# Performance work log

Hardware: AMD Instinct MI355X
Metric: run time of the kernel (lower is better)

The kernel has to match this reference:

```python
import jax, jax.numpy as jnp
import numpy as np

EPS = 1e-06


def setup_inputs() -> dict:
    key = jax.random.key(0)
    ks = jax.random.split(key, 8)
    B, L, n, C = 4, 4096, 4, 1024
    D = n * C
    x = jax.random.normal(ks[0], (B, L, n, C), dtype=jnp.float32)
    # learned params (phi_* are zero-init in the module; use small random for a
    # non-trivial correctness baseline)
    norm_w = jnp.ones((D,), dtype=jnp.float32)
    W_pre = 0.02 * jax.random.normal(ks[1], (n, D), dtype=jnp.float32)
    W_post = 0.02 * jax.random.normal(ks[2], (n, D), dtype=jnp.float32)
    W_res = 0.02 * jax.random.normal(ks[3], (n * n, D), dtype=jnp.float32)
    b_pre = jnp.ones((n,), dtype=jnp.float32) / n
    b_post = jnp.ones((n,), dtype=jnp.float32)
    b_res = jnp.zeros((n, n), dtype=jnp.float32)
    alpha_pre = jnp.float32(0.01)
    alpha_post = jnp.float32(0.01)
    alpha_res = jnp.float32(0.01)
    return {"x": x, "norm_w": norm_w, "W_pre": W_pre, "W_post": W_post,
            "W_res": W_res, "b_pre": b_pre, "b_post": b_post, "b_res": b_res,
            "alpha_pre": alpha_pre, "alpha_post": alpha_post, "alpha_res": alpha_res}


def _cayley(M):
    # M: [N, n, n] -> orthogonal Q = (I - S)^{-1} (I + S), S skew-symmetric part
    S = 0.5 * (M - jnp.swapaxes(M, -1, -2))
    I = jnp.eye(M.shape[-1], dtype=M.dtype)
    return jnp.linalg.solve(I - S, I + S)


def reference(x, norm_w, W_pre, W_post, W_res, b_pre, b_post, b_res,
              alpha_pre, alpha_post, alpha_res):
    B, L, n, C = x.shape
    xf = x.reshape(B * L, n * C)
    # RMSNorm over n*C
    rms = jnp.sqrt(jnp.mean(xf * xf, axis=-1, keepdims=True) + EPS)
    xn = (xf / rms) * norm_w
    # tiny projections
    H_pre = jax.nn.sigmoid(alpha_pre * (xn @ W_pre.T) + b_pre)          # [BL, n]
    H_post = 2.0 * jax.nn.sigmoid(alpha_post * (xn @ W_post.T) + b_post)  # [BL, n]
    M = (alpha_res * (xn @ W_res.T)).reshape(B * L, n, n) + b_res
    H_res = _cayley(M).reshape(B, L, n, n)
    H_pre = H_pre.reshape(B, L, n)
    H_post = H_post.reshape(B, L, n)
    # pre-mapping: aggregate streams -> [B, L, C]
    y = jnp.einsum('bln,blnc->blc', H_pre, x)
    z = y  # identity sublayer
    # post-mapping: distribute back to streams
    o = H_post[..., None] * z[:, :, None, :]                             # [B,L,n,C]
    # residual mapping: orthogonal stream mixing
    r = jnp.einsum('blmn,blnc->blmc', H_res, x)
    return r + o
```

## Files before the change

### kernel.cpp

```cpp
#include <hip/hip_runtime.h>
#include <math.h>

#define DTOT   4096
#define NTOK   16384
#define NJ     24
#define NG     25
#define DC     256
#define NCHUNK (DTOT / DC)
#define TOKB   256

__global__ void prep_kernel(const float* __restrict__ Wpre,
                            const float* __restrict__ Wpost,
                            const float* __restrict__ Wres,
                            const float* __restrict__ nw,
                            float* __restrict__ Wt) {
    int i = blockIdx.x * 256 + threadIdx.x;
    if (i >= DTOT * NJ) return;
    int d = i / NJ;
    int j = i - d * NJ;
    float w;
    if (j < 4)       w = Wpre [(size_t)j       * DTOT + d];
    else if (j < 8)  w = Wpost[(size_t)(j - 4) * DTOT + d];
    else             w = Wres [(size_t)(j - 8) * DTOT + d];
    Wt[i] = w * nw[d];
}

__global__ __launch_bounds__(256) void dots_kernel(
        const float* __restrict__ x,
        const float* __restrict__ Wt,
        float* __restrict__ Gpart) {
    __shared__ float wlds[DC * NJ];

    const int tid = threadIdx.x;
    const int tg  = blockIdx.x;
    const int ch  = blockIdx.y;

    {
        const float4* src = (const float4*)(Wt + (size_t)ch * DC * NJ);
        float4* dst = (float4*)wlds;
        #pragma unroll
        for (int i = 0; i < (DC * NJ / 4) / 256; ++i)
            dst[tid + 256 * i] = src[tid + 256 * i];
    }
    __syncthreads();

    const int tok = tg * TOKB + tid;
    const float4* __restrict__ x0 =
        (const float4*)(x + (size_t)tok * DTOT + (size_t)ch * DC);

    float acc[NG];
    #pragma unroll
    for (int j = 0; j < NG; ++j) acc[j] = 0.f;

    for (int dd4 = 0; dd4 < DC / 4; ++dd4) {
        float4 r = x0[dd4];
        float a[4] = { r.x, r.y, r.z, r.w };
        #pragma unroll
        for (int k = 0; k < 4; ++k) {
            const float xa = a[k];
            const float4* __restrict__ wv =
                (const float4*)(wlds + (dd4 * 4 + k) * NJ);
            #pragma unroll
            for (int jv = 0; jv < 6; ++jv) {
                const float4 w = wv[jv];
                acc[4*jv+0] += xa * w.x;
                acc[4*jv+1] += xa * w.y;
                acc[4*jv+2] += xa * w.z;
                acc[4*jv+3] += xa * w.w;
            }
            acc[NG-1] += xa * xa;
        }
    }

    float* gp = Gpart + (size_t)ch * NG * NTOK;
    #pragma unroll
    for (int j = 0; j < NG; ++j)
        gp[(size_t)j * NTOK + tok] = acc[j];
}

__global__ __launch_bounds__(256) void out_kernel(
        const float* __restrict__ x,
        const float* __restrict__ Gpart,
        const float* __restrict__ bpre,
        const float* __restrict__ bpost,
        const float* __restrict__ bres,
        const float* __restrict__ apre,
        const float* __restrict__ apost,
        const float* __restrict__ ares,
        float* __restrict__ out) {
    const int lane  = threadIdx.x & 63;
    const int token = blockIdx.x * 4 + (threadIdx.x >> 6);

    float s = 0.f;
    if (lane < NG) {
        const float* gp = Gpart + (size_t)lane * NTOK + token;
        #pragma unroll
        for (int c = 0; c < NCHUNK; ++c)
            s += gp[(size_t)c * NG * NTOK];
    }

    float g[NG];
    #pragma unroll
    for (int j = 0; j < NG; ++j) g[j] = __shfl(s, j, 64);

    const float inv = rsqrtf(g[NG-1] * (1.0f / DTOT) + 1e-6f);
    const float a_pre  = apre[0];
    const float a_post = apost[0];
    const float a_res  = ares[0];

    float hpre[4], hpost[4];
    #pragma unroll
    for (int i = 0; i < 4; ++i) {
        float z1 = a_pre  * g[i]     * inv + bpre[i];
        hpre[i]  = 1.f / (1.f + expf(-z1));
        float z2 = a_post * g[4 + i] * inv + bpost[i];
        hpost[i] = 2.f / (1.f + expf(-z2));
    }

    float M[4][4];
    #pragma unroll
    for (int i = 0; i < 4; ++i)
        #pragma unroll
        for (int j = 0; j < 4; ++j)
            M[i][j] = a_res * g[8 + i * 4 + j] * inv + bres[i * 4 + j];

    float A[4][8];
    #pragma unroll
    for (int i = 0; i < 4; ++i)
        #pragma unroll
        for (int j = 0; j < 4; ++j) {
            float S = 0.5f * (M[i][j] - M[j][i]);
            float I = (i == j) ? 1.f : 0.f;
            A[i][j]     = I - S;
            A[i][4 + j] = I + S;
        }
    #pragma unroll
    for (int k = 0; k < 4; ++k) {
        float pv = 1.f / A[k][k];
        #pragma unroll
        for (int c = 0; c < 8; ++c) A[k][c] *= pv;
        #pragma unroll
        for (int i = 0; i < 4; ++i) {
            if (i == k) continue;
            float f = A[i][k];
            #pragma unroll
            for (int c = 0; c < 8; ++c) A[i][c] -= f * A[k][c];
        }
    }
    float cf[16];
    #pragma unroll
    for (int m = 0; m < 4; ++m)
        #pragma unroll
        for (int n = 0; n < 4; ++n)
            cf[m * 4 + n] = A[m][4 + n] + hpost[m] * hpre[n];

    const float* xt = x + (size_t)token * DTOT;
    float* ot = out + (size_t)token * DTOT;

    #pragma unroll
    for (int cc = 0; cc < 4; ++cc) {
        const int c0 = cc * 256 + lane * 4;
        float4 xv[4];
        #pragma unroll
        for (int n = 0; n < 4; ++n)
            xv[n] = *(const float4*)(xt + n * 1024 + c0);
        #pragma unroll
        for (int m = 0; m < 4; ++m) {
            float4 o;
            o.x = cf[m*4+0] * xv[0].x; o.y = cf[m*4+0] * xv[0].y;
            o.z = cf[m*4+0] * xv[0].z; o.w = cf[m*4+0] * xv[0].w;
            #pragma unroll
            for (int n = 1; n < 4; ++n) {
                const float c = cf[m * 4 + n];
                o.x += c * xv[n].x;
                o.y += c * xv[n].y;
                o.z += c * xv[n].z;
                o.w += c * xv[n].w;
            }
            *(float4*)(ot + m * 1024 + c0) = o;
        }
    }
}

extern "C" void kernel_launch(void* const* d_in, const int* in_sizes, int n_in,
                              void* d_out, int out_size, void* d_ws, size_t ws_size,
                              hipStream_t stream) {
    const float* x     = (const float*)d_in[0];
    const float* nw    = (const float*)d_in[1];
    const float* Wpre  = (const float*)d_in[2];
    const float* Wpost = (const float*)d_in[3];
    const float* Wres  = (const float*)d_in[4];
    const float* bpre  = (const float*)d_in[5];
    const float* bpost = (const float*)d_in[6];
    const float* bres  = (const float*)d_in[7];
    const float* apre  = (const float*)d_in[8];
    const float* apost = (const float*)d_in[9];
    const float* ares  = (const float*)d_in[10];
    float* out = (float*)d_out;

    float* Wt    = (float*)d_ws;
    float* Gpart = (float*)((char*)d_ws + (size_t)DTOT * NJ * sizeof(float));

    prep_kernel<<<(DTOT * NJ + 255) / 256, 256, 0, stream>>>(Wpre, Wpost, Wres, nw, Wt);

    dim3 ga(NTOK / TOKB, NCHUNK);
    dots_kernel<<<ga, 256, 0, stream>>>(x, Wt, Gpart);

    out_kernel<<<NTOK / 4, 256, 0, stream>>>(x, Gpart, bpre, bpost, bres,
                                             apre, apost, ares, out);
}
```

Before: 593.5 us.

## Compute two tokens per thread in dots kernel with prefetch and larger out blocks

The dots kernel now has each thread accumulate projections for two tokens, so every LDS weight load feeds twice as many FMAs. It also prefetches the next x vectors one step ahead, and uses a smaller feature chunk with a larger token block. The out kernel runs 16 tokens per 1024-thread block and switches to fast __expf. The smaller chunk doubles the number of partial sums written to and reduced from Gpart, which grows workspace and reduction traffic. The extra accumulators add register pressure.

```diff
diff --git a/kernel.cpp b/kernel.cpp
--- a/kernel.cpp
+++ b/kernel.cpp
@@ -5,9 +5,9 @@
 #define NTOK   16384
 #define NJ     24
 #define NG     25
-#define DC     256
+#define DC     128
 #define NCHUNK (DTOT / DC)
-#define TOKB   256
+#define TOKB   512
 
 __global__ void prep_kernel(const float* __restrict__ Wpre,
                             const float* __restrict__ Wpost,
@@ -25,7 +25,7 @@
     Wt[i] = w * nw[d];
 }
 
-__global__ __launch_bounds__(256) void dots_kernel(
+__global__ __launch_bounds__(256, 4) void dots_kernel(
         const float* __restrict__ x,
         const float* __restrict__ Wt,
         float* __restrict__ Gpart) {
@@ -44,41 +44,62 @@
     }
     __syncthreads();
 
-    const int tok = tg * TOKB + tid;
+    const int tok0 = tg * TOKB + tid;
+    const int tok1 = tok0 + 256;
     const float4* __restrict__ x0 =
-        (const float4*)(x + (size_t)tok * DTOT + (size_t)ch * DC);
-
-    float acc[NG];
-    #pragma unroll
-    for (int j = 0; j < NG; ++j) acc[j] = 0.f;
-
-    for (int dd4 = 0; dd4 < DC / 4; ++dd4) {
-        float4 r = x0[dd4];
-        float a[4] = { r.x, r.y, r.z, r.w };
-        #pragma unroll
-        for (int k = 0; k < 4; ++k) {
-            const float xa = a[k];
+        (const float4*)(x + (size_t)tok0 * DTOT + (size_t)ch * DC);
+    const float4* __restrict__ x1 =
+        (const float4*)(x + (size_t)tok1 * DTOT + (size_t)ch * DC);
+
+    float pa[NG], pb[NG];
+    #pragma unroll
+    for (int j = 0; j < NG; ++j) { pa[j] = 0.f; pb[j] = 0.f; }
+
+    float4 a0 = x0[0], a1 = x0[1];
+    float4 b0 = x1[0], b1 = x1[1];
+
+    for (int g = 0; g < DC / 8; ++g) {
+        float4 na0 = a0, na1 = a1, nb0 = b0, nb1 = b1;
+        if (g < DC / 8 - 1) {
+            na0 = x0[2 * g + 2];
+            na1 = x0[2 * g + 3];
+            nb0 = x1[2 * g + 2];
+            nb1 = x1[2 * g + 3];
+        }
+
+        const float xs[8] = { a0.x, a0.y, a0.z, a0.w, a1.x, a1.y, a1.z, a1.w };
+        const float ys[8] = { b0.x, b0.y, b0.z, b0.w, b1.x, b1.y, b1.z, b1.w };
+
+        #pragma unroll
+        for (int k = 0; k < 8; ++k) {
+            const float xa = xs[k];
+            const float xb = ys[k];
             const float4* __restrict__ wv =
-                (const float4*)(wlds + (dd4 * 4 + k) * NJ);
+                (const float4*)(wlds + (g * 8 + k) * NJ);
             #pragma unroll
             for (int jv = 0; jv < 6; ++jv) {
                 const float4 w = wv[jv];
-                acc[4*jv+0] += xa * w.x;
-                acc[4*jv+1] += xa * w.y;
-                acc[4*jv+2] += xa * w.z;
-                acc[4*jv+3] += xa * w.w;
+                pa[4*jv+0] += xa * w.x;  pb[4*jv+0] += xb * w.x;
+                pa[4*jv+1] += xa * w.y;  pb[4*jv+1] += xb * w.y;
+                pa[4*jv+2] += xa * w.z;  pb[4*jv+2] += xb * w.z;
+                pa[4*jv+3] += xa * w.w;  pb[4*jv+3] += xb * w.w;
             }
-            acc[NG-1] += xa * xa;
-        }
+            pa[NG-1] += xa * xa;
+            pb[NG-1] += xb * xb;
+        }
+
+        a0 = na0; a1 = na1; b0 = nb0; b1 = nb1;
     }
 
     float* gp = Gpart + (size_t)ch * NG * NTOK;
     #pragma unroll
-    for (int j = 0; j < NG; ++j)
-        gp[(size_t)j * NTOK + tok] = acc[j];
-}
-
-__global__ __launch_bounds__(256) void out_kernel(
+    for (int j = 0; j < NG; ++j) {
+        gp[(size_t)j * NTOK + tok0] = pa[j];
+        gp[(size_t)j * NTOK + tok1] = pb[j];
+    }
+}
+
+__global__ __launch_bounds__(1024) void out_kernel(
         const float* __restrict__ x,
         const float* __restrict__ Gpart,
         const float* __restrict__ bpre,
@@ -89,7 +110,7 @@
         const float* __restrict__ ares,
         float* __restrict__ out) {
     const int lane  = threadIdx.x & 63;
-    const int token = blockIdx.x * 4 + (threadIdx.x >> 6);
+    const int token = blockIdx.x * 16 + (threadIdx.x >> 6);
 
     float s = 0.f;
     if (lane < NG) {
@@ -112,9 +133,9 @@
     #pragma unroll
     for (int i = 0; i < 4; ++i) {
         float z1 = a_pre  * g[i]     * inv + bpre[i];
-        hpre[i]  = 1.f / (1.f + expf(-z1));
+        hpre[i]  = 1.f / (1.f + __expf(-z1));
         float z2 = a_post * g[4 + i] * inv + bpost[i];
-        hpost[i] = 2.f / (1.f + expf(-z2));
+        hpost[i] = 2.f / (1.f + __expf(-z2));
     }
 
     float M[4][4];
@@ -206,6 +227,6 @@
     dim3 ga(NTOK / TOKB, NCHUNK);
     dots_kernel<<<ga, 256, 0, stream>>>(x, Wt, Gpart);
 
-    out_kernel<<<NTOK / 4, 256, 0, stream>>>(x, Gpart, bpre, bpost, bres,
-                                             apre, apost, ares, out);
-}
+    out_kernel<<<NTOK / 16, 1024, 0, stream>>>(x, Gpart, bpre, bpost, bres,
+                                               apre, apost, ares, out);
+}
```

After: 673.0 us. +13.4%, slower.

## Coalesce x reads in dots kernel via 8-lane split per token and reverse out order

Applied to the files above, without the earlier changes.

The dots kernel now gives each token to 8 lanes that read contiguous float4 slices of x, with a j-major weight layout in LDS, a one-ahead register prefetch and a shuffle-xor reduction. Previously each thread streamed its own token row with strided accesses. The output kernel uses 1024-thread blocks and walks tokens in reverse, so it starts on the most recently read x data while that is still in cache. It also switches to fast __expf. The costs are more blocks and LDS reloads per block, plus the shuffle reduction.

```diff
diff --git a/kernel.cpp b/kernel.cpp
--- a/kernel.cpp
+++ b/kernel.cpp
@@ -7,78 +7,93 @@
 #define NG     25
 #define DC     256
 #define NCHUNK (DTOT / DC)
-#define TOKB   256
+#define TPB    32
 
 __global__ void prep_kernel(const float* __restrict__ Wpre,
                             const float* __restrict__ Wpost,
                             const float* __restrict__ Wres,
                             const float* __restrict__ nw,
-                            float* __restrict__ Wt) {
+                            float* __restrict__ Wtj) {
     int i = blockIdx.x * 256 + threadIdx.x;
-    if (i >= DTOT * NJ) return;
-    int d = i / NJ;
-    int j = i - d * NJ;
+    if (i >= NJ * DTOT) return;
+    int j = i / DTOT;
+    int d = i - j * DTOT;
     float w;
-    if (j < 4)       w = Wpre [(size_t)j       * DTOT + d];
-    else if (j < 8)  w = Wpost[(size_t)(j - 4) * DTOT + d];
-    else             w = Wres [(size_t)(j - 8) * DTOT + d];
-    Wt[i] = w * nw[d];
-}
-
-__global__ __launch_bounds__(256) void dots_kernel(
+    if (j < 4)       w = Wpre [i];
+    else if (j < 8)  w = Wpost[i - 4 * DTOT];
+    else             w = Wres [i - 8 * DTOT];
+    Wtj[i] = w * nw[d];
+}
+
+__global__ __launch_bounds__(256, 5) void dots_kernel(
         const float* __restrict__ x,
-        const float* __restrict__ Wt,
+        const float* __restrict__ Wtj,
         float* __restrict__ Gpart) {
-    __shared__ float wlds[DC * NJ];
+    __shared__ float wlds[NJ * DC];
 
     const int tid = threadIdx.x;
-    const int tg  = blockIdx.x;
     const int ch  = blockIdx.y;
 
     {
-        const float4* src = (const float4*)(Wt + (size_t)ch * DC * NJ);
+        const float4* src = (const float4*)Wtj;
         float4* dst = (float4*)wlds;
         #pragma unroll
-        for (int i = 0; i < (DC * NJ / 4) / 256; ++i)
-            dst[tid + 256 * i] = src[tid + 256 * i];
+        for (int r = 0; r < 6; ++r) {
+            int idx = r * 256 + tid;
+            int j = idx >> 6;
+            int f = idx & 63;
+            dst[idx] = src[(size_t)j * (DTOT / 4) + ch * (DC / 4) + f];
+        }
     }
     __syncthreads();
 
-    const int tok = tg * TOKB + tid;
-    const float4* __restrict__ x0 =
-        (const float4*)(x + (size_t)tok * DTOT + (size_t)ch * DC);
+    const int w    = tid >> 6;
+    const int lane = tid & 63;
+    const int t8   = lane >> 3;
+    const int dp   = lane & 7;
+    const int tok  = blockIdx.x * TPB + w * 8 + t8;
+
+    const float4* __restrict__ xp =
+        (const float4*)(x + (size_t)tok * DTOT + ch * DC);
+    const float4* __restrict__ wl4 = (const float4*)wlds;
 
     float acc[NG];
     #pragma unroll
     for (int j = 0; j < NG; ++j) acc[j] = 0.f;
 
-    for (int dd4 = 0; dd4 < DC / 4; ++dd4) {
-        float4 r = x0[dd4];
-        float a[4] = { r.x, r.y, r.z, r.w };
-        #pragma unroll
-        for (int k = 0; k < 4; ++k) {
-            const float xa = a[k];
-            const float4* __restrict__ wv =
-                (const float4*)(wlds + (dd4 * 4 + k) * NJ);
-            #pragma unroll
-            for (int jv = 0; jv < 6; ++jv) {
-                const float4 w = wv[jv];
-                acc[4*jv+0] += xa * w.x;
-                acc[4*jv+1] += xa * w.y;
-                acc[4*jv+2] += xa * w.z;
-                acc[4*jv+3] += xa * w.w;
-            }
-            acc[NG-1] += xa * xa;
-        }
-    }
-
-    float* gp = Gpart + (size_t)ch * NG * NTOK;
-    #pragma unroll
-    for (int j = 0; j < NG; ++j)
-        gp[(size_t)j * NTOK + tok] = acc[j];
-}
-
-__global__ __launch_bounds__(256) void out_kernel(
+    float4 xv = xp[dp];
+    #pragma unroll
+    for (int i = 0; i < 8; ++i) {
+        float4 nx = xv;
+        if (i < 7) nx = xp[(i + 1) * 8 + dp];
+        const int base = i * 8 + dp;
+        #pragma unroll
+        for (int j = 0; j < NJ; ++j) {
+            const float4 w4 = wl4[j * 64 + base];
+            acc[j] += xv.x * w4.x + xv.y * w4.y + xv.z * w4.z + xv.w * w4.w;
+        }
+        acc[NG - 1] += xv.x * xv.x + xv.y * xv.y + xv.z * xv.z + xv.w * xv.w;
+        xv = nx;
+    }
+
+    #pragma unroll
+    for (int j = 0; j < NG; ++j) {
+        float v = acc[j];
+        v += __shfl_xor(v, 1, 64);
+        v += __shfl_xor(v, 2, 64);
+        v += __shfl_xor(v, 4, 64);
+        acc[j] = v;
+    }
+
+    if (dp == 0) {
+        float* gp = Gpart + (size_t)ch * NG * NTOK + tok;
+        #pragma unroll
+        for (int j = 0; j < NG; ++j)
+            gp[(size_t)j * NTOK] = acc[j];
+    }
+}
+
+__global__ __launch_bounds__(1024) void out_kernel(
         const float* __restrict__ x,
         const float* __restrict__ Gpart,
         const float* __restrict__ bpre,
@@ -89,7 +104,7 @@
         const float* __restrict__ ares,
         float* __restrict__ out) {
     const int lane  = threadIdx.x & 63;
-    const int token = blockIdx.x * 4 + (threadIdx.x >> 6);
+    const int token = (NTOK - 16 - blockIdx.x * 16) + (threadIdx.x >> 6);
 
     float s = 0.f;
     if (lane < NG) {
@@ -112,9 +127,9 @@
     #pragma unroll
     for (int i = 0; i < 4; ++i) {
         float z1 = a_pre  * g[i]     * inv + bpre[i];
-        hpre[i]  = 1.f / (1.f + expf(-z1));
+        hpre[i]  = 1.f / (1.f + __expf(-z1));
         float z2 = a_post * g[4 + i] * inv + bpost[i];
-        hpost[i] = 2.f / (1.f + expf(-z2));
+        hpost[i] = 2.f / (1.f + __expf(-z2));
     }
 
     float M[4][4];
@@ -198,14 +213,14 @@
     const float* ares  = (const float*)d_in[10];
     float* out = (float*)d_out;
 
-    float* Wt    = (float*)d_ws;
-    float* Gpart = (float*)((char*)d_ws + (size_t)DTOT * NJ * sizeof(float));
-
-    prep_kernel<<<(DTOT * NJ + 255) / 256, 256, 0, stream>>>(Wpre, Wpost, Wres, nw, Wt);
-
-    dim3 ga(NTOK / TOKB, NCHUNK);
-    dots_kernel<<<ga, 256, 0, stream>>>(x, Wt, Gpart);
-
-    out_kernel<<<NTOK / 4, 256, 0, stream>>>(x, Gpart, bpre, bpost, bres,
-                                             apre, apost, ares, out);
-}
+    float* Wtj   = (float*)d_ws;
+    float* Gpart = (float*)((char*)d_ws + (size_t)NJ * DTOT * sizeof(float));
+
+    prep_kernel<<<(NJ * DTOT + 255) / 256, 256, 0, stream>>>(Wpre, Wpost, Wres, nw, Wtj);
+
+    dim3 ga(NTOK / TPB, NCHUNK);
+    dots_kernel<<<ga, 256, 0, stream>>>(x, Wtj, Gpart);
+
+    out_kernel<<<NTOK / 16, 1024, 0, stream>>>(x, Gpart, bpre, bpost, bres,
+                                               apre, apost, ares, out);
+}
```

Result: faster. 566.1 us (-4.6%).
